# Kernel optimization log

Hardware: AMD Instinct MI355X
Metric: run time of the kernel (lower is better)

## Reference

```python
import jax, jax.numpy as jnp
import numpy as np

OUT_H, OUT_W = 14, 14
SPATIAL_SCALE = 0.25

def setup_inputs() -> dict:
    key = jax.random.key(0)
    k1, k2, k3, k4, k5, k6 = jax.random.split(key, 6)
    B, C, H, W = 2, 256, 200, 336
    R = 1000
    features = jax.random.normal(k1, (B, C, H, W), jnp.float32)
    img_h, img_w = H / SPATIAL_SCALE, W / SPATIAL_SCALE
    cx = jax.random.uniform(k2, (R,)) * img_w
    cy = jax.random.uniform(k3, (R,)) * img_h
    bw = jax.random.uniform(k4, (R,)) * 256.0 + 16.0
    bh = jax.random.uniform(k5, (R,)) * 256.0 + 16.0
    x1 = jnp.clip(cx - bw / 2, 0.0, img_w - 1.0)
    x2 = jnp.clip(cx + bw / 2, 0.0, img_w - 1.0)
    y1 = jnp.clip(cy - bh / 2, 0.0, img_h - 1.0)
    y2 = jnp.clip(cy + bh / 2, 0.0, img_h - 1.0)
    bidx = jax.random.randint(k6, (R,), 0, B).astype(jnp.float32)
    rois = jnp.stack([bidx, x1, y1, x2, y2], axis=1)  # (R, 5)
    return {"features": features, "rois": rois}

def _roi_align(features, rois):
    # features: (B, C, H, W); rois: (R, 5) = (batch_idx, x1, y1, x2, y2) in image coords
    B, C, H, W = features.shape
    R = rois.shape[0]
    b = jax.lax.stop_gradient(rois[:, 0]).astype(jnp.int32)
    x1, y1, x2, y2 = rois[:, 1], rois[:, 2], rois[:, 3], rois[:, 4]
    # bin-center grid in [0,1] (affine_grid identity, align_corners=False, then normalized)
    gx = (jnp.arange(OUT_W, dtype=features.dtype) + 0.5) / OUT_W
    gy = (jnp.arange(OUT_H, dtype=features.dtype) + 0.5) / OUT_H
    px = x1[:, None] + gx[None, :] * (x2 - x1)[:, None]  # (R, OUT_W) abs image x
    py = y1[:, None] + gy[None, :] * (y2 - y1)[:, None]  # (R, OUT_H) abs image y
    # grid_sample(align_corners=False) with normalized coord abs/(size/scale): pix = abs*scale - 0.5
    fx = jnp.broadcast_to(px[:, None, :], (R, OUT_H, OUT_W)) * SPATIAL_SCALE - 0.5
    fy = jnp.broadcast_to(py[:, :, None], (R, OUT_H, OUT_W)) * SPATIAL_SCALE - 0.5
    x0 = jnp.floor(fx); y0 = jnp.floor(fy)
    lx = fx - x0; ly = fy - y0
    x0i = x0.astype(jnp.int32); y0i = y0.astype(jnp.int32)
    feats_flat = features.reshape(B, C, H * W)
    bb = b[:, None, None]  # (R,1,1)
    def corner(yi, xi):
        valid = ((xi >= 0) & (xi < W) & (yi >= 0) & (yi < H)).astype(features.dtype)
        idx = jnp.clip(yi, 0, H - 1) * W + jnp.clip(xi, 0, W - 1)  # (R,OUT_H,OUT_W)
        v = feats_flat[bb, :, idx]  # (R, OUT_H, OUT_W, C)
        return v * valid[..., None]  # zeros padding_mode
    v00 = corner(y0i, x0i)
    v01 = corner(y0i, x0i + 1)
    v10 = corner(y0i + 1, x0i)
    v11 = corner(y0i + 1, x0i + 1)
    wx0 = (1.0 - lx)[..., None]; wx1 = lx[..., None]
    wy0 = (1.0 - ly)[..., None]; wy1 = ly[..., None]
    out = wy0 * (wx0 * v00 + wx1 * v01) + wy1 * (wx0 * v10 + wx1 * v11)
    return out.transpose(0, 3, 1, 2)  # (R, C, OUT_H, OUT_W)

def reference(features, rois):
    return _roi_align(features, rois)
```

## Files before the change

kernel.cpp:

```cpp
#include <hip/hip_runtime.h>

constexpr int B = 2, C = 256, H = 200, W = 336;
constexpr int HW = H * W;
constexpr int OH = 14, OW = 14, OHW = OH * OW;
constexpr float SCALE = 0.25f;

constexpr int CSPLIT = 4;
constexpr int CPB = C / CSPLIT;

typedef float f2 __attribute__((ext_vector_type(2), aligned(4)));

__global__ __launch_bounds__(256) void roi_align_kernel(
    const float* __restrict__ feat,
    const float* __restrict__ rois,
    float* __restrict__ out)
{
    const int r   = blockIdx.x;
    const int c0  = blockIdx.y * CPB;
    const int tid = threadIdx.x;

    const float* roi = rois + r * 5;
    const float bf = roi[0];
    const float x1 = roi[1], y1 = roi[2], x2 = roi[3], y2 = roi[4];
    const int b = __builtin_amdgcn_readfirstlane((int)bf);

    const int s = tid;
    if (s >= OHW) return;

    const int oh = s / OW;
    const int ow = s - oh * OW;

    const float fx = (x1 + (ow + 0.5f) * (1.0f / OW) * (x2 - x1)) * SCALE - 0.5f;
    const float fy = (y1 + (oh + 0.5f) * (1.0f / OH) * (y2 - y1)) * SCALE - 0.5f;

    const float x0f = floorf(fx), y0f = floorf(fy);
    const float lx = fx - x0f,   ly = fy - y0f;
    const int x0 = (int)x0f,  y0 = (int)y0f;
    const int x1i = x0 + 1,   y1i = y0 + 1;

    const float cxw0 = ((x0  >= 0 && x0  < W) ? 1.0f : 0.0f) * (1.0f - lx);
    const float cxw1 = ((x1i >= 0 && x1i < W) ? 1.0f : 0.0f) * lx;
    const float ryw0 = ((y0  >= 0 && y0  < H) ? 1.0f : 0.0f) * (1.0f - ly);
    const float ryw1 = ((y1i >= 0 && y1i < H) ? 1.0f : 0.0f) * ly;

    const int px = min(max(x0, 0), W - 2);
    const bool swp = (x0 != px);
    const float wxa = swp ? cxw1 : cxw0;
    const float wxb = swp ? cxw0 : cxw1;
    const float a0 = ryw0 * wxa, b0 = ryw0 * wxb;
    const float a1 = ryw1 * wxa, b1 = ryw1 * wxb;

    const int cy0 = min(max(y0,  0), H - 1);
    const int cy1 = min(max(y1i, 0), H - 1);
    const int i0 = cy0 * W + px;
    const int i1 = cy1 * W + px;

    const float* p  = feat + (size_t)(b * C + c0) * HW;
    float*       op = out  + (size_t)r * C * OHW + (size_t)c0 * OHW + s;

    #pragma unroll 8
    for (int c = 0; c < CPB; ++c) {
        const f2 r0 = *reinterpret_cast<const f2*>(p + i0);
        const f2 r1 = *reinterpret_cast<const f2*>(p + i1);
        *op = fmaf(a0, r0.x, fmaf(b0, r0.y, fmaf(a1, r1.x, b1 * r1.y)));
        p  += HW;
        op += OHW;
    }
}

extern "C" void kernel_launch(void* const* d_in, const int* in_sizes, int n_in,
                              void* d_out, int out_size, void* d_ws, size_t ws_size,
                              hipStream_t stream) {
    const float* feat = (const float*)d_in[0];
    const float* rois = (const float*)d_in[1];
    float* out = (float*)d_out;

    const int R = in_sizes[1] / 5;
    dim3 grid(R, CSPLIT);
    dim3 block(256);
    roi_align_kernel<<<grid, block, 0, stream>>>(feat, rois, out);
}
```

Baseline: 437.5 us.

## Sort ROIs by spatial locality and map sorted groups to XCDs for L2 reuse

Adds a single-block bitonic sort that orders ROIs by batch index, y-band and x-center. The main kernel becomes a 1D grid in which consecutive blocks round-robin across the 8 XCDs, so each XCD works on a contiguous, spatially sorted chunk of ROIs across all channel slices. The intent is to raise reuse of overlapping feature regions in each XCD's L2 cache and cut HBM traffic. It adds an extra kernel launch and a serial dependency, hardcodes R=1000, and assumes blocks are dispatched round-robin across XCDs.

```diff
diff --git a/kernel.cpp b/kernel.cpp
--- a/kernel.cpp
+++ b/kernel.cpp
@@ -4,20 +4,63 @@
 constexpr int HW = H * W;
 constexpr int OH = 14, OW = 14, OHW = OH * OW;
 constexpr float SCALE = 0.25f;
+constexpr int R = 1000;
 
 constexpr int CSPLIT = 4;
 constexpr int CPB = C / CSPLIT;
+constexpr int NXCD = 8;
+constexpr int RPX = R / NXCD;
 
 typedef float f2 __attribute__((ext_vector_type(2), aligned(4)));
+
+__global__ __launch_bounds__(1024) void sort_rois_kernel(
+    const float* __restrict__ rois, int* __restrict__ order)
+{
+    __shared__ unsigned key[1024];
+    const int t = threadIdx.x;
+
+    unsigned k = 0xFFFFFFFFu;
+    if (t < R) {
+        const float* roi = rois + t * 5;
+        const int   b  = (int)roi[0];
+        const float cx = 0.5f * (roi[1] + roi[3]);
+        const float cy = 0.5f * (roi[2] + roi[4]);
+        const int yb   = min(12, max(0, (int)cy >> 6));
+        const int band = (b << 4) | yb;
+        const int cxi  = min(2047, max(0, (int)cx));
+        k = ((unsigned)band << 21) | ((unsigned)cxi << 10) | (unsigned)t;
+    }
+    key[t] = k;
+
+    for (int size = 2; size <= 1024; size <<= 1) {
+        for (int stride = size >> 1; stride > 0; stride >>= 1) {
+            __syncthreads();
+            const int j = t ^ stride;
+            if (j > t) {
+                const bool up = ((t & size) == 0);
+                const unsigned a = key[t], b2 = key[j];
+                if ((a > b2) == up) { key[t] = b2; key[j] = a; }
+            }
+        }
+    }
+    __syncthreads();
+    if (t < R) order[t] = (int)(key[t] & 1023u);
+}
 
 __global__ __launch_bounds__(256) void roi_align_kernel(
     const float* __restrict__ feat,
     const float* __restrict__ rois,
+    const int*  __restrict__ order,
     float* __restrict__ out)
 {
-    const int r   = blockIdx.x;
-    const int c0  = blockIdx.y * CPB;
-    const int tid = threadIdx.x;
+    const int bid   = blockIdx.x;
+    const int xcd   = bid & (NXCD - 1);
+    const int slot  = bid >> 3;
+    const int slice = slot & (CSPLIT - 1);
+    const int rank  = slot >> 2;
+    const int r     = order[xcd * RPX + rank];
+    const int c0    = slice * CPB;
+    const int tid   = threadIdx.x;
 
     const float* roi = rois + r * 5;
     const float bf = roi[0];
@@ -74,9 +117,11 @@
     const float* feat = (const float*)d_in[0];
     const float* rois = (const float*)d_in[1];
     float* out = (float*)d_out;
+    int* order = (int*)d_ws;
 
-    const int R = in_sizes[1] / 5;
-    dim3 grid(R, CSPLIT);
+    sort_rois_kernel<<<1, 1024, 0, stream>>>(rois, order);
+
+    dim3 grid(R * CSPLIT);
     dim3 block(256);
-    roi_align_kernel<<<grid, block, 0, stream>>>(feat, rois, out);
+    roi_align_kernel<<<grid, block, 0, stream>>>(feat, rois, order, out);
 }
```

New measurement: 413.0 us. -5.6%, faster.
